# Kernel optimization log

Hardware: AMD Instinct MI355X
Metric: run time of the kernel (lower is better)

Reference implementation:

```python
import jax, jax.numpy as jnp
import numpy as np

B, L, ENC, DEC, EMB, ATT, V, T = 64, 196, 2048, 512, 512, 512, 20000, 26


def setup_inputs() -> dict:
    key = jax.random.key(0)
    ks = jax.random.split(key, 24)
    W = lambda i, shape: (jax.random.normal(ks[i], shape, dtype=jnp.float32) * 0.02)
    inp = {
        'encoder_output': jax.random.normal(ks[0], (B, L, ENC), dtype=jnp.float32),
        'caption': jax.random.randint(ks[1], (B, T), 0, V),
        'caption_lengths': jax.random.randint(ks[2], (B,), 2, T + 1),
        # embedding (uniform(-0.1,0.1) as in init_weights)
        'embed_W': jax.random.uniform(ks[3], (V, EMB), jnp.float32, -0.1, 0.1),
        # attention
        'We': W(4, (ENC, ATT)), 'be': jnp.zeros((ATT,), jnp.float32),
        'Wd': W(5, (DEC, ATT)), 'bd': jnp.zeros((ATT,), jnp.float32),
        'Wa': W(6, (ATT,)),     'ba': jnp.zeros((), jnp.float32),
        # LSTMCell (i,f,g,o order)
        'Wih': W(7, (4 * DEC, ENC + EMB)), 'bih': jnp.zeros((4 * DEC,), jnp.float32),
        'Whh': W(8, (4 * DEC, DEC)),       'bhh': jnp.zeros((4 * DEC,), jnp.float32),
        # gating + state init + output fc
        'Wfb': W(9, (DEC, ENC)),  'bfb': jnp.zeros((ENC,), jnp.float32),
        'Wh0': W(10, (ENC, DEC)), 'bh0': jnp.zeros((DEC,), jnp.float32),
        'Wc0': W(11, (ENC, DEC)), 'bc0': jnp.zeros((DEC,), jnp.float32),
        'Wfc': jax.random.uniform(ks[12], (DEC, V), jnp.float32, -0.1, 0.1),
        'bfc': jnp.zeros((V,), jnp.float32),
    }
    return inp


def _forward(encoder_output, caption, caption_lengths, embed_W, We, be, Wd, bd,
             Wa, ba, Wih, bih, Whh, bhh, Wfb, bfb, Wh0, bh0, Wc0, bc0, Wfc, bfc):
    # sort batch by descending caption length (as in the torch code)
    sort_ind = jnp.argsort(-caption_lengths)
    enc = encoder_output[sort_ind]          # [B, L, ENC]
    cap = caption[sort_ind]                 # [B, T]
    lens = caption_lengths[sort_ind] - 1    # decode steps per row

    emb = embed_W[cap]                      # [B, T, EMB]
    mean = enc.mean(axis=1)
    h0 = jnp.tanh(mean @ Wh0 + bh0)         # [B, DEC]
    c0 = jnp.tanh(mean @ Wc0 + bc0)
    enc_att = enc @ We + be                 # [B, L, ATT] (precomputed once)

    Tm1 = cap.shape[1] - 1
    # mask[t, b] = row b still active at step t
    mask = (jnp.arange(Tm1)[:, None] < lens[None, :]).astype(enc.dtype)  # [T-1, B]
    emb_steps = jnp.swapaxes(emb[:, :Tm1], 0, 1)                          # [T-1, B, EMB]

    def step(carry, x):
        h, c = carry
        e_t, m = x                                    # [B, EMB], [B]
        dec_att = h @ Wd + bd                         # [B, ATT]
        u = jnp.tanh(enc_att + dec_att[:, None, :])   # [B, L, ATT]
        scores = u @ Wa + ba                          # [B, L]
        alpha = jax.nn.softmax(scores, axis=1)
        z = jnp.einsum('bl,ble->be', alpha, enc)      # context [B, ENC]
        gate = jax.nn.sigmoid(h @ Wfb + bfb)          # [B, ENC]
        inp = jnp.concatenate([e_t, gate * z], axis=1)
        g = inp @ Wih.T + bih + h @ Whh.T + bhh       # [B, 4*DEC]
        i, f, gg, o = jnp.split(g, 4, axis=1)
        c_new = jax.nn.sigmoid(f) * c + jax.nn.sigmoid(i) * jnp.tanh(gg)
        h_new = jax.nn.sigmoid(o) * jnp.tanh(c_new)
        pred = h_new @ Wfc + bfc                      # [B, V]  (deep_output_layer == fc(h))
        return (h_new, c_new), (pred * m[:, None], alpha * m[:, None])

    _, (preds, alphas) = jax.lax.scan(step, (h0, c0), (emb_steps, mask))
    preds = jnp.swapaxes(preds, 0, 1)    # [B, T-1, V]
    alphas = jnp.swapaxes(alphas, 0, 1)  # [B, T-1, L]
    return preds, alphas, cap, lens


def reference(encoder_output, caption, caption_lengths, embed_W, We, be, Wd, bd,
              Wa, ba, Wih, bih, Whh, bhh, Wfb, bfb, Wh0, bh0, Wc0, bc0, Wfc, bfc):
    return _forward(encoder_output, caption, caption_lengths, embed_W, We, be, Wd, bd,
                    Wa, ba, Wih, bih, Whh, bhh, Wfb, bfb, Wh0, bh0, Wc0, bc0, Wfc, bfc)
```

## Files before the change

kernel.cpp:

```cpp
#include <hip/hip_runtime.h>
#include <hip/hip_bf16.h>

#define BB 64
#define LL 196
#define ENC 2048
#define DEC 512
#define EMB 512
#define ATT 512
#define VV 20000
#define TT 26
#define TM1 25

typedef __attribute__((ext_vector_type(8))) short bf16x8;
typedef __attribute__((ext_vector_type(4))) short bf16x4;
typedef __attribute__((ext_vector_type(4))) float f32x4;

#define MFMA16(a,b,c) __builtin_amdgcn_mfma_f32_16x16x32_bf16(a,b,c,0,0,0)

typedef const __attribute__((address_space(1))) void g_void;
typedef __attribute__((address_space(3))) void l_void;

__device__ __forceinline__ void stage16(const void* g, void* l){
    __builtin_amdgcn_global_load_lds((g_void*)g, (l_void*)l, 16, 0, 0);
}

#define WAITV(N) asm volatile("s_waitcnt vmcnt(" #N ")" ::: "memory")
#define PHASE_SYNC() do { __builtin_amdgcn_s_barrier(); __builtin_amdgcn_sched_barrier(0); } while(0)

__device__ __forceinline__ float tanh_fast(float x){
    float ax = fabsf(x);
    float e  = __expf(-2.f*ax);
    float r  = (1.f - e)/(1.f + e);
    return x >= 0.f ? r : -r;
}
__device__ __forceinline__ float sigmoidf_(float x){
    return 1.f/(1.f + __expf(-x));
}
__device__ __forceinline__ short f2bf(float v){
    __hip_bfloat16 b = __float2bfloat16(v);
    return __builtin_bit_cast(short, b);
}
__device__ __forceinline__ float bf2f(short s){
    __hip_bfloat16 b = __builtin_bit_cast(__hip_bfloat16, s);
    return __bfloat162float(b);
}

__global__ void k_sort(const int* __restrict__ clen, const int* __restrict__ cap,
                       const float* __restrict__ bih, const float* __restrict__ bhh,
                       int* __restrict__ sind, int* __restrict__ lens_s,
                       float* __restrict__ bsum,
                       float* __restrict__ out_cap, float* __restrict__ out_lens)
{
    int i = threadIdx.x;
    int li = clen[i];
    int r = 0;
    for (int j = 0; j < BB; j++){
        int lj = clen[j];
        r += (lj > li) || (lj == li && j < i);
    }
    sind[r] = i;
    lens_s[r] = li - 1;
    out_lens[r] = (float)(li - 1);
    for (int t = 0; t < TT; t++)
        out_cap[r*TT + t] = (float)cap[i*TT + t];
    for (int j = i; j < 4*DEC; j += BB)
        bsum[j] = bih[j] + bhh[j];
}

struct PrepArgs {
    const float* enc; const int* sind; short* enc_s;
    const float* Wfc; short* Wfcb;
    const float* Wih; const float* Whh; short* Bg;
    const float* We;  short* Web;
    const float* Wfb; short* Bfb;
    const float* Wd;  short* Wdp;
    float* mean;
    const float* embW; const int* cap; short* embs;
    int fast; int blkoff;
};

#define SEG0 12544
#define SEG1 (SEG0 + 5000)
#define SEG2 (SEG1 + 2560)
#define SEG3 (SEG2 + 512)
#define SEG4 (SEG3 + 512)
#define SEG5 (SEG4 + 512)
#define SEG6 (SEG5 + 512)
#define SEG7 (SEG6 + 1600)
#define SEG8 (SEG7 + 128)

__device__ __forceinline__ void pack_frag(int idx, const float* src, int ld,
                                          int K, int N, short* dst,
                                          int ktOff, int ntOff, int ntTot, bool NK)
{
    int ntCnt = N >> 4, ktCnt = K >> 5;
    int lane = idx & 63, rest = idx >> 6;
    if (rest >= ktCnt*ntCnt) return;
    int nt = rest % ntCnt, kt = rest / ntCnt;
    int k = kt*32 + (lane>>4)*8, n = nt*16 + (lane&15);
    bf16x8 v;
    #pragma unroll
    for (int j = 0; j < 8; j++){
        float f = NK ? src[(size_t)n*ld + k + j] : src[(size_t)(k+j)*ld + n];
        v[j] = f2bf(f);
    }
    *(bf16x8*)(dst + ((size_t)((kt+ktOff)*ntTot + (nt+ntOff))*64 + lane)*8) = v;
}

__launch_bounds__(256)
__global__ void k_prep(PrepArgs P)
{
    int blk = blockIdx.x + P.blkoff, tid = threadIdx.x;
    if (blk < SEG0){
        if (!P.fast) return;
        size_t idx = ((size_t)blk*256 + tid)*8;
        int r = (int)(idx / (LL*ENC));
        size_t rem = idx - (size_t)r*(LL*ENC);
        const float* s = P.enc + (size_t)P.sind[r]*(LL*ENC) + rem;
        bf16x8 v;
        float4 f0 = *(const float4*)s, f1 = *(const float4*)(s+4);
        v[0]=f2bf(f0.x); v[1]=f2bf(f0.y); v[2]=f2bf(f0.z); v[3]=f2bf(f0.w);
        v[4]=f2bf(f1.x); v[5]=f2bf(f1.y); v[6]=f2bf(f1.z); v[7]=f2bf(f1.w);
        *(bf16x8*)(P.enc_s + idx) = v;
    } else if (blk < SEG1){
        pack_frag((blk-SEG0)*256 + tid, P.Wfc, VV, 512, VV, P.Wfcb, 0, 0, 1250, false);
    } else if (blk < SEG2){
        pack_frag((blk-SEG1)*256 + tid, P.Wih, 2560, 2560, 2048, P.Bg, 0, 0, 128, true);
    } else if (blk < SEG3){
        pack_frag((blk-SEG2)*256 + tid, P.We, ATT, ENC, ATT, P.Web, 0, 0, 32, false);
    } else if (blk < SEG4){
        pack_frag((blk-SEG3)*256 + tid, P.Wfb, ENC, 512, 2048, P.Bfb, 0, 0, 128, false);
    } else if (blk < SEG5){
        pack_frag((blk-SEG4)*256 + tid, P.Whh, 512, 512, 2048, P.Bg, 80, 0, 128, true);
    } else if (blk < SEG6){
        int rel = blk - SEG5;
        int b = rel >> 3;
        int e = (rel & 7)*256 + tid;
        int sb = P.sind[b];
        const float* p = P.enc + ((size_t)sb*LL)*ENC + e;
        float s = 0.f;
        for (int l = 0; l < LL; l++) s += p[(size_t)l*ENC];
        P.mean[b*ENC + e] = s * (1.f/(float)LL);
    } else if (blk < SEG7){
        int rel = blk - SEG6;
        int b = rel / 25, t = rel % 25;
        int token = P.cap[P.sind[b]*TT + t];
        const float* src = P.embW + (size_t)token*EMB + tid*2;
        unsigned u = (unsigned)(unsigned short)f2bf(src[0]) |
                     ((unsigned)(unsigned short)f2bf(src[1]) << 16);
        ((unsigned*)(P.embs + ((size_t)b*TM1 + t)*EMB))[tid] = u;
    } else if (blk < SEG8){
        pack_frag((blk-SEG7)*256 + tid, P.Wd, ATT, 512, 512, P.Wdp, 0, 0, 32, false);
    }
}

#define KT 32
__launch_bounds__(256)
__global__ void k_h0part(const float* __restrict__ A1, const float* __restrict__ B1,
                         const float* __restrict__ B2, float* __restrict__ hpart)
{
    __shared__ float As[KT][64];
    __shared__ float Bs[KT][64];
    const int tid = threadIdx.x;
    const int n0  = blockIdx.x*64;
    const int kq  = blockIdx.y;
    float acc[4][4] = {};
    const int lrow = tid >> 3, lcol = tid & 7;
    const int bn = (tid & 15)*4, bk = tid >> 4;
    const int bi0 = (tid >> 4)*4, nj0 = (tid & 15)*4;
    for (int k0 = kq*256; k0 < kq*256 + 256; k0 += KT){
        #pragma unroll
        for (int p = 0; p < 2; p++){
            int m = lrow + p*32;
            float4 v = *(const float4*)(A1 + (size_t)m*2048 + k0 + lcol*4);
            As[lcol*4+0][m] = v.x; As[lcol*4+1][m] = v.y;
            As[lcol*4+2][m] = v.z; As[lcol*4+3][m] = v.w;
        }
        {
            bool hi = (n0 >= 512);
            const float* B = hi ? B2 : B1;
            int ncol = n0 - (hi ? 512 : 0) + bn;
            #pragma unroll
            for (int p = 0; p < 2; p++){
                int k = bk + p*16;
                *(float4*)&Bs[k][bn] = *(const float4*)(B + (size_t)(k0+k)*512 + ncol);
            }
        }
        __syncthreads();
        #pragma unroll
        for (int k = 0; k < KT; k++){
            const float4 av = *(const float4*)&As[k][bi0];
            const float4 bv = *(const float4*)&Bs[k][nj0];
            acc[0][0] += av.x*bv.x; acc[0][1] += av.x*bv.y; acc[0][2] += av.x*bv.z; acc[0][3] += av.x*bv.w;
            acc[1][0] += av.y*bv.x; acc[1][1] += av.y*bv.y; acc[1][2] += av.y*bv.z; acc[1][3] += av.y*bv.w;
            acc[2][0] += av.z*bv.x; acc[2][1] += av.z*bv.y; acc[2][2] += av.z*bv.z; acc[2][3] += av.z*bv.w;
            acc[3][0] += av.w*bv.x; acc[3][1] += av.w*bv.y; acc[3][2] += av.w*bv.z; acc[3][3] += av.w*bv.w;
        }
        __syncthreads();
    }
    #pragma unroll
    for (int i = 0; i < 4; i++)
        #pragma unroll
        for (int j = 0; j < 4; j++){
            int b = bi0 + i, n = n0 + nj0 + j;
            hpart[((size_t)kq*64 + b)*1024 + n] = acc[i][j];
        }
}

__global__ void k_h0fin(const float* __restrict__ hpart, const float* __restrict__ bh0,
                        const float* __restrict__ bc0, short* __restrict__ h0,
                        float* __restrict__ c)
{
    int idx = blockIdx.x*256 + threadIdx.x;
    int b = idx >> 10, n = idx & 1023;
    float v = (n < 512) ? bh0[n] : bc0[n-512];
    for (int kq = 0; kq < 8; kq++) v += hpart[((size_t)kq*64 + b)*1024 + n];
    float r = tanh_fast(v);
    if (n < 512) h0[b*512 + n] = f2bf(r);
    else         c[b*512 + (n-512)] = r;
}

template<bool BF16SRC>
__launch_bounds__(256)
__global__ void k_encatt_mfma(const void* __restrict__ encp, const int* __restrict__ sind,
                              const short* __restrict__ Web, const float* __restrict__ be,
                              short* __restrict__ enc_att)
{
    __shared__ short As[64*32];
    int tid = threadIdx.x, wv = tid>>6, lane = tid&63;
    int hi = lane>>4, lo = lane&15;
    int m0 = blockIdx.x*64;
    int ntbase = blockIdx.y*8 + wv*2;
    int srow = tid>>2, schunk = tid&3;
    const short* gsrcB = nullptr; const float* gsrcF = nullptr;
    if (BF16SRC){
        gsrcB = (const short*)encp + (size_t)(m0+srow)*ENC + schunk*8;
    } else {
        int grow = m0 + srow;
        int b = grow/LL, l = grow - b*LL;
        gsrcF = (const float*)encp + ((size_t)sind[b]*LL + l)*ENC + schunk*8;
    }
    int sws = srow*32 + (schunk ^ ((srow>>1)&3))*8;
    f32x4 acc[2][4] = {};
    for (int kt = 0; kt < 64; kt++){
        bf16x8 v;
        if (BF16SRC){
            v = *(const bf16x8*)(gsrcB + kt*32);
        } else {
            float4 f0 = *(const float4*)(gsrcF + kt*32);
            float4 f1 = *(const float4*)(gsrcF + kt*32 + 4);
            v[0]=f2bf(f0.x); v[1]=f2bf(f0.y); v[2]=f2bf(f0.z); v[3]=f2bf(f0.w);
            v[4]=f2bf(f1.x); v[5]=f2bf(f1.y); v[6]=f2bf(f1.z); v[7]=f2bf(f1.w);
        }
        __syncthreads();
        *(bf16x8*)(As + sws) = v;
        __syncthreads();
        bf16x8 af[4];
        #pragma unroll
        for (int m = 0; m < 4; m++){
            int r = m*16 + lo;
            af[m] = *(const bf16x8*)(As + r*32 + (hi ^ ((r>>1)&3))*8);
        }
        #pragma unroll
        for (int n = 0; n < 2; n++){
            bf16x8 b = *(const bf16x8*)(Web + ((size_t)(kt*32 + ntbase + n)*64 + lane)*8);
            #pragma unroll
            for (int m = 0; m < 4; m++)
                acc[n][m] = MFMA16(af[m], b, acc[n][m]);
        }
    }
    #pragma unroll
    for (int n = 0; n < 2; n++)
        #pragma unroll
        for (int m = 0; m < 4; m++)
            #pragma unroll
            for (int j = 0; j < 4; j++){
                int row = m0 + m*16 + hi*4 + j;
                int col = (ntbase + n)*16 + lo;
                enc_att[(size_t)row*ATT + col] = f2bf(acc[n][m][j] + be[col]);
            }
}

__launch_bounds__(256)
__global__ void k_hgemm(const short* __restrict__ h_in, const short* __restrict__ Wdp,
                        const short* __restrict__ Bfb,
                        const float* __restrict__ bd, const float* __restrict__ bfb,
                        float* __restrict__ dg, float* __restrict__ gateb)
{
    __shared__ short ring[4*16384];
    int tid = threadIdx.x, wv = tid>>6, lane = tid&63;
    int hi = lane>>4, lo = lane&15;
    int gw = blockIdx.x*4 + wv;
    bool isdg = (gw < 32);
    int ntl  = isdg ? gw : gw - 32;
    int bstr = isdg ? 32 : 128;
    const short* Bp = isdg ? Wdp : Bfb;
    int srow = tid>>2;
    int swc  = (tid&3) ^ ((srow>>1)&3);
    int swz  = (hi ^ ((lo>>1)&3))*8;
    auto STG = [&](int q){
        short* buf = ring + q*16384;
        #pragma unroll
        for (int j = 0; j < 4; j++){
            int kt = 4*q + j;
            stage16(h_in + (size_t)srow*512 + kt*32 + swc*8,
                    buf + j*2048 + wv*512);
            stage16(Bp + ((size_t)(kt*bstr + ntl)*64 + lane)*8,
                    buf + 8192 + wv*2048 + j*512);
        }
    };
    STG(0); STG(1); STG(2);
    f32x4 acc[4] = {};
    auto CMP = [&](int pp){
        const short* buf = ring + pp*16384;
        #pragma unroll
        for (int j = 0; j < 4; j++){
            bf16x8 b = *(const bf16x8*)(buf + 8192 + wv*2048 + j*512 + lane*8);
            const short* Ab = buf + j*2048;
            #pragma unroll
            for (int m = 0; m < 4; m++){
                bf16x8 a = *(const bf16x8*)(Ab + (m*16 + lo)*32 + swz);
                acc[m] = MFMA16(a, b, acc[m]);
            }
        }
    };
    WAITV(16); PHASE_SYNC(); STG(3); CMP(0);
    WAITV(16); PHASE_SYNC(); CMP(1);
    WAITV(8);  PHASE_SYNC(); CMP(2);
    WAITV(0);  PHASE_SYNC(); CMP(3);
    int col = ntl*16 + lo;
    if (isdg){
        #pragma unroll
        for (int m = 0; m < 4; m++)
            #pragma unroll
            for (int j = 0; j < 4; j++)
                dg[(m*16 + hi*4 + j)*512 + col] = acc[m][j] + bd[col];
    } else {
        #pragma unroll
        for (int m = 0; m < 4; m++)
            #pragma unroll
            for (int j = 0; j < 4; j++)
                gateb[(m*16 + hi*4 + j)*2048 + col] = sigmoidf_(acc[m][j] + bfb[col]);
    }
}

__launch_bounds__(512)
__global__ void k_attnz(const float* __restrict__ dg, const short* __restrict__ encat,
                        const float* __restrict__ Wa, const float* __restrict__ ba,
                        const short* __restrict__ embs, const float* __restrict__ gateb,
                        const short* __restrict__ enc_s, const float* __restrict__ enc,
                        const int* __restrict__ sind, const int* __restrict__ lens_s,
                        short* __restrict__ inp, float* __restrict__ out_alphas,
                        int t, int fast)
{
    __shared__ float da[512];
    __shared__ float was[512];
    __shared__ float sc[200];
    __shared__ float red[16];
    __shared__ float al[200];
    __shared__ float zpart[4*2048];
    int b = blockIdx.x, tid = threadIdx.x;
    int lane = tid & 63, wv = tid >> 6;
    da[tid] = dg[b*512 + tid];
    was[tid] = Wa[tid];
    __syncthreads();
    float ba_v = ba[0];
    for (int l = wv; l < LL; l += 8){
        const short* ea = encat + ((size_t)b*LL + l)*ATT;
        float s = 0.f;
        #pragma unroll
        for (int q = 0; q < 8; q++){
            int a = lane + q*64;
            s += tanh_fast(bf2f(ea[a]) + da[a]) * was[a];
        }
        #pragma unroll
        for (int off = 32; off; off >>= 1) s += __shfl_xor(s, off);
        if (lane == 0) sc[l] = s + ba_v;
    }
    __syncthreads();
    float v = -1e30f, e = 0.f;
    if (tid < 256){
        v = (tid < LL) ? sc[tid] : -1e30f;
        float mx = v;
        #pragma unroll
        for (int off = 32; off; off >>= 1) mx = fmaxf(mx, __shfl_xor(mx, off));
        if (lane == 0) red[wv] = mx;
    }
    if (tid < 256){
        const unsigned* s32 = (const unsigned*)(embs + ((size_t)b*TM1 + t)*EMB);
        ((unsigned*)(inp + (size_t)b*2560))[tid] = s32[tid];
    }
    __syncthreads();
    float mxa = fmaxf(fmaxf(red[0], red[1]), fmaxf(red[2], red[3]));
    if (tid < 256){
        e = (tid < LL) ? __expf(v - mxa) : 0.f;
        float sm = e;
        #pragma unroll
        for (int off = 32; off; off >>= 1) sm += __shfl_xor(sm, off);
        if (lane == 0) red[8 + wv] = sm;
    }
    __syncthreads();
    float tot = red[8] + red[9] + red[10] + red[11];
    if (tid < LL){
        float alv = e / tot;
        al[tid] = alv;
        float m = (t < lens_s[b]) ? 1.f : 0.f;
        out_alphas[((size_t)b*TM1 + t)*LL + tid] = alv * m;
    }
    __syncthreads();
    {
        int ls = tid >> 7;
        int cs = tid & 127;
        int c0 = cs*16;
        float a16[16] = {};
        if (fast){
            const short* base = enc_s + ((size_t)b*LL)*ENC + c0;
            for (int l = ls; l < LL; l += 4){
                float av = al[l];
                const short* r = base + (size_t)l*ENC;
                bf16x8 v0 = *(const bf16x8*)(r);
                bf16x8 v1 = *(const bf16x8*)(r + 8);
                #pragma unroll
                for (int j = 0; j < 8; j++){
                    a16[j]     += av*bf2f(v0[j]);
                    a16[8 + j] += av*bf2f(v1[j]);
                }
            }
        } else {
            const float* base = enc + ((size_t)sind[b]*LL)*ENC + c0;
            for (int l = ls; l < LL; l += 4){
                float av = al[l];
                const float* r = base + (size_t)l*ENC;
                float4 f0 = *(const float4*)(r),     f1 = *(const float4*)(r+4);
                float4 f2 = *(const float4*)(r + 8), f3 = *(const float4*)(r+12);
                a16[0]+=av*f0.x; a16[1]+=av*f0.y; a16[2]+=av*f0.z; a16[3]+=av*f0.w;
                a16[4]+=av*f1.x; a16[5]+=av*f1.y; a16[6]+=av*f1.z; a16[7]+=av*f1.w;
                a16[8]+=av*f2.x; a16[9]+=av*f2.y; a16[10]+=av*f2.z; a16[11]+=av*f2.w;
                a16[12]+=av*f3.x; a16[13]+=av*f3.y; a16[14]+=av*f3.z; a16[15]+=av*f3.w;
            }
        }
        float* zp = zpart + ls*2048 + c0;
        #pragma unroll
        for (int jj = 0; jj < 16; jj++){
            int slot = (jj + cs) & 15;
            zp[slot] = a16[slot];
        }
    }
    __syncthreads();
    {
        int c = tid*4;
        const float* gt = gateb + (size_t)b*2048 + c;
        bf16x4 o;
        #pragma unroll
        for (int j = 0; j < 4; j++){
            float s = zpart[0*2048 + c + j] + zpart[1*2048 + c + j]
                    + zpart[2*2048 + c + j] + zpart[3*2048 + c + j];
            o[j] = f2bf(gt[j] * s);
        }
        *(bf16x4*)(inp + (size_t)b*2560 + 512 + c) = o;
    }
}

__launch_bounds__(512)
__global__ void k_glstm(const short* __restrict__ inp, const short* __restrict__ h_in,
                        const short* __restrict__ Bg, const float* __restrict__ bsum,
                        float* __restrict__ c, short* __restrict__ h_out)
{
    __shared__ short ring[3*24576];
    float* gs = (float*)ring;
    int tid = threadIdx.x, wv = tid>>6, lane = tid&63;
    int hi = lane>>4, lo = lane&15;
    int gate = wv & 3, khalf = wv >> 2;
    int j16 = blockIdx.x;
    int nt = gate*32 + j16;
    int sl   = tid >> 8;
    int st   = tid & 255;
    int srow = st >> 2;
    int swc  = (st&3) ^ ((srow>>1)&3);
    int swz  = (hi ^ ((lo>>1)&3))*8;
    auto STG = [&](int q){
        short* buf = ring + (q%3)*24576;
        #pragma unroll
        for (int j = 0; j < 3; j++){
            int kt = sl*48 + 3*q + j;
            const short* src;
            if (kt < 80) src = inp  + (size_t)srow*2560 + kt*32 + swc*8;
            else         src = h_in + (size_t)srow*512  + (kt-80)*32 + swc*8;
            stage16(src, buf + (sl*3 + j)*2048 + (wv&3)*512);
            int ktw = khalf*48 + 3*q + j;
            stage16(Bg + ((size_t)(ktw*128 + nt)*64 + lane)*8,
                    buf + 12288 + wv*1536 + j*512);
        }
    };
    STG(0); STG(1);
    f32x4 acc[4] = {};
    auto CMP = [&](int pp){
        const short* buf = ring + (pp%3)*24576;
        #pragma unroll
        for (int j = 0; j < 3; j++){
            bf16x8 b = *(const bf16x8*)(buf + 12288 + wv*1536 + j*512 + lane*8);
            const short* Ab = buf + (khalf*3 + j)*2048;
            #pragma unroll
            for (int m = 0; m < 4; m++){
                bf16x8 a = *(const bf16x8*)(Ab + (m*16 + lo)*32 + swz);
                acc[m] = MFMA16(a, b, acc[m]);
            }
        }
    };
    for (int pp = 0; pp < 14; pp++){
        WAITV(6); PHASE_SYNC();
        STG(pp + 2);
        CMP(pp);
    }
    WAITV(6); PHASE_SYNC(); CMP(14);
    WAITV(0); PHASE_SYNC(); CMP(15);
    __syncthreads();
    #pragma unroll
    for (int m = 0; m < 4; m++)
        #pragma unroll
        for (int j = 0; j < 4; j++)
            gs[wv*1088 + (m*16 + hi*4 + j)*17 + lo] = acc[m][j];
    __syncthreads();
    #pragma unroll
    for (int rep = 0; rep < 2; rep++){
        int idx = rep*512 + tid;
        int row = idx >> 4, cl = idx & 15;
        int col = j16*16 + cl;
        float s0 = gs[0*1088 + row*17 + cl] + gs[4*1088 + row*17 + cl] + bsum[col];
        float s1 = gs[1*1088 + row*17 + cl] + gs[5*1088 + row*17 + cl] + bsum[512 + col];
        float s2 = gs[2*1088 + row*17 + cl] + gs[6*1088 + row*17 + cl] + bsum[1024 + col];
        float s3 = gs[3*1088 + row*17 + cl] + gs[7*1088 + row*17 + cl] + bsum[1536 + col];
        int ci = row*512 + col;
        float cn = sigmoidf_(s1)*c[ci] + sigmoidf_(s0)*tanh_fast(s2);
        c[ci] = cn;
        h_out[ci] = f2bf(sigmoidf_(s3)*tanh_fast(cn));
    }
}

__launch_bounds__(256)
__global__ void k_predall(const short* __restrict__ hh, const short* __restrict__ Wfcb,
                          const float* __restrict__ bfc, const int* __restrict__ lens_s,
                          float* __restrict__ out_preds)
{
    __shared__ short ring[4*2048];
    int tid = threadIdx.x, wv = tid>>6, lane = tid&63;
    int hi = lane>>4, lo = lane&15;
    int nt = blockIdx.x*4 + wv;
    if (nt > 1249) nt = 1249;
    int mt0 = blockIdx.y*5;
    bf16x8 breg[16];
    #pragma unroll
    for (int kt = 0; kt < 16; kt++)
        breg[kt] = *(const bf16x8*)(Wfcb + ((size_t)(kt*1250 + nt)*64 + lane)*8);
    int col = nt*16 + lo;
    float bv = bfc[col];
    int lv[16];
    #pragma unroll
    for (int m = 0; m < 4; m++)
        #pragma unroll
        for (int j = 0; j < 4; j++)
            lv[m*4 + j] = lens_s[m*16 + hi*4 + j];

    int srow = tid>>2;
    int swc  = (tid&3) ^ ((srow>>1)&3);
    int swz  = (hi ^ ((lo>>1)&3))*8;
    const short* hh0 = hh + (size_t)(mt0 + 1)*(BB*DEC);
    auto STG = [&](int q){
        const short* src = hh0 + (size_t)(q>>4)*(BB*DEC) + (size_t)srow*512
                         + (q&15)*32 + swc*8;
        stage16(src, ring + (q&3)*2048 + wv*512);
    };
    STG(0); STG(1); STG(2);

    auto CMP = [&](f32x4* acc, int kt, int pp){
        const short* base = ring + (pp&3)*2048;
        #pragma unroll
        for (int m = 0; m < 4; m++){
            bf16x8 a = *(const bf16x8*)(base + (m*16 + lo)*32 + swz);
            acc[m] = MFMA16(a, breg[kt], acc[m]);
        }
    };
    auto STORE = [&](f32x4* acc, int mta){
        #pragma unroll
        for (int m = 0; m < 4; m++)
            #pragma unroll
            for (int j = 0; j < 4; j++){
                int row = m*16 + hi*4 + j;
                float mk = (mta < lv[m*4 + j]) ? 1.f : 0.f;
                out_preds[((size_t)row*TM1 + mta)*VV + col] = mk*(acc[m][j] + bv);
            }
    };

    for (int mt = 0; mt < 4; mt++){
        f32x4 acc[4] = {};
        #pragma unroll
        for (int kt = 0; kt < 16; kt++){
            int pp = mt*16 + kt;
            WAITV(2); PHASE_SYNC();
            STG(pp + 3);
            CMP(acc, kt, pp);
        }
        STORE(acc, mt0 + mt);
    }
    {
        f32x4 acc[4] = {};
        #pragma unroll
        for (int kt = 0; kt < 13; kt++){
            int pp = 64 + kt;
            WAITV(2); PHASE_SYNC();
            if (pp < 77) STG(pp + 3);
            CMP(acc, kt, pp);
        }
        WAITV(2); PHASE_SYNC(); CMP(acc, 13, 77);
        WAITV(1); PHASE_SYNC(); CMP(acc, 14, 78);
        WAITV(0); PHASE_SYNC(); CMP(acc, 15, 79);
        STORE(acc, mt0 + 4);
    }
}

extern "C" void kernel_launch(void* const* d_in, const int* in_sizes, int n_in,
                              void* d_out, int out_size, void* d_ws, size_t ws_size,
                              hipStream_t stream)
{
    const float* enc  = (const float*)d_in[0];
    const int*   cap  = (const int*)  d_in[1];
    const int*   clen = (const int*)  d_in[2];
    const float* embW = (const float*)d_in[3];
    const float* We   = (const float*)d_in[4];
    const float* be   = (const float*)d_in[5];
    const float* Wd   = (const float*)d_in[6];
    const float* bd   = (const float*)d_in[7];
    const float* Wa   = (const float*)d_in[8];
    const float* ba   = (const float*)d_in[9];
    const float* Wih  = (const float*)d_in[10];
    const float* bih  = (const float*)d_in[11];
    const float* Whh  = (const float*)d_in[12];
    const float* bhh  = (const float*)d_in[13];
    const float* Wfb  = (const float*)d_in[14];
    const float* bfb  = (const float*)d_in[15];
    const float* Wh0  = (const float*)d_in[16];
    const float* bh0  = (const float*)d_in[17];
    const float* Wc0  = (const float*)d_in[18];
    const float* bc0  = (const float*)d_in[19];
    const float* Wfc  = (const float*)d_in[20];
    const float* bfc  = (const float*)d_in[21];

    char* w = (char*)d_ws;
    size_t cur = 0;
    auto alloc = [&](size_t bytes)->char*{
        char* p = w + cur; cur = (cur + bytes + 255) & ~(size_t)255; return p;
    };
    int*   sind   = (int*)  alloc(256);
    int*   lens_s = (int*)  alloc(256);
    float* bsum   = (float*)alloc(4*DEC*4);
    float* mean   = (float*)alloc(BB*ENC*4);
    float* hpart  = (float*)alloc((size_t)8*64*1024*4);
    float* c      = (float*)alloc(BB*DEC*4);
    short* hh     = (short*)alloc((size_t)(TM1+1)*BB*DEC*2);
    float* dg     = (float*)alloc(BB*512*4);
    float* gateb  = (float*)alloc(BB*2048*4);
    short* inp    = (short*)alloc(BB*2560*2);
    short* embs   = (short*)alloc((size_t)BB*TM1*EMB*2);
    short* Wdp    = (short*)alloc((size_t)512*512*2);
    short* Web    = (short*)alloc((size_t)ENC*ATT*2);
    short* Bfb    = (short*)alloc((size_t)512*2048*2);
    short* Bg     = (short*)alloc((size_t)3072*2048*2);
    short* Wfcb   = (short*)alloc((size_t)512*VV*2);
    short* encat  = (short*)alloc((size_t)BB*LL*ATT*2);
    short* enc_s  = (short*)alloc((size_t)BB*LL*ENC*2);
    bool fast = (ws_size >= cur);
    int fastI = fast ? 1 : 0;

    float* out        = (float*)d_out;
    float* out_preds  = out;
    float* out_alphas = out + 32000000ull;
    float* out_cap    = out + 32313600ull;
    float* out_lens   = out + 32315264ull;

    k_sort<<<1, 64, 0, stream>>>(clen, cap, bih, bhh, sind, lens_s, bsum,
                                 out_cap, out_lens);
    PrepArgs P;
    P.enc = enc; P.sind = sind; P.enc_s = enc_s;
    P.Wfc = Wfc; P.Wfcb = Wfcb;
    P.Wih = Wih; P.Whh = Whh; P.Bg = Bg;
    P.We = We; P.Web = Web;
    P.Wfb = Wfb; P.Bfb = Bfb;
    P.Wd = Wd; P.Wdp = Wdp;
    P.mean = mean;
    P.embW = embW; P.cap = cap; P.embs = embs;
    P.fast = fastI;
    P.blkoff = 0;
    k_prep<<<SEG0, 256, 0, stream>>>(P);
    PrepArgs P2 = P;
    P2.blkoff = SEG0;
    k_prep<<<SEG8 - SEG0, 256, 0, stream>>>(P2);

    k_h0part<<<dim3(16, 8), 256, 0, stream>>>(mean, Wh0, Wc0, hpart);
    k_h0fin<<<256, 256, 0, stream>>>(hpart, bh0, bc0, hh, c);

    if (fast)
        k_encatt_mfma<true ><<<dim3(196, 4), 256, 0, stream>>>(enc_s, sind, Web, be, encat);
    else
        k_encatt_mfma<false><<<dim3(196, 4), 256, 0, stream>>>(enc,   sind, Web, be, encat);

    for (int t = 0; t < TM1; t++){
        const short* h_in  = hh + (size_t)t*(BB*DEC);
        short*       h_out = hh + (size_t)(t+1)*(BB*DEC);
        k_hgemm<<<40, 256, 0, stream>>>(h_in, Wdp, Bfb, bd, bfb, dg, gateb);
        k_attnz<<<64, 512, 0, stream>>>(dg, encat, Wa, ba, embs, gateb, enc_s, enc,
                                        sind, lens_s, inp, out_alphas, t, fastI);
        k_glstm<<<32, 512, 0, stream>>>(inp, h_in, Bg, bsum, c, h_out);
    }
    k_predall<<<dim3(313, 5), 256, 0, stream>>>(hh, Wfcb, bfc, lens_s, out_preds);
}
```

Before: 1.856 ms.

## Fuse per-step decoder and gate GEMMs into attention kernel, dropping k_hgemm

```diff
diff --git a/kernel.cpp b/kernel.cpp
--- a/kernel.cpp
+++ b/kernel.cpp
@@ -72,8 +72,6 @@
     const float* Wfc; short* Wfcb;
     const float* Wih; const float* Whh; short* Bg;
     const float* We;  short* Web;
-    const float* Wfb; short* Bfb;
-    const float* Wd;  short* Wdp;
     float* mean;
     const float* embW; const int* cap; short* embs;
     int fast; int blkoff;
@@ -85,9 +83,7 @@
 #define SEG3 (SEG2 + 512)
 #define SEG4 (SEG3 + 512)
 #define SEG5 (SEG4 + 512)
-#define SEG6 (SEG5 + 512)
-#define SEG7 (SEG6 + 1600)
-#define SEG8 (SEG7 + 128)
+#define SEG6 (SEG5 + 1600)
 
 __device__ __forceinline__ void pack_frag(int idx, const float* src, int ld,
                                           int K, int N, short* dst,
@@ -129,11 +125,9 @@
     } else if (blk < SEG3){
         pack_frag((blk-SEG2)*256 + tid, P.We, ATT, ENC, ATT, P.Web, 0, 0, 32, false);
     } else if (blk < SEG4){
-        pack_frag((blk-SEG3)*256 + tid, P.Wfb, ENC, 512, 2048, P.Bfb, 0, 0, 128, false);
+        pack_frag((blk-SEG3)*256 + tid, P.Whh, 512, 512, 2048, P.Bg, 80, 0, 128, true);
     } else if (blk < SEG5){
-        pack_frag((blk-SEG4)*256 + tid, P.Whh, 512, 512, 2048, P.Bg, 80, 0, 128, true);
-    } else if (blk < SEG6){
-        int rel = blk - SEG5;
+        int rel = blk - SEG4;
         int b = rel >> 3;
         int e = (rel & 7)*256 + tid;
         int sb = P.sind[b];
@@ -141,16 +135,14 @@
         float s = 0.f;
         for (int l = 0; l < LL; l++) s += p[(size_t)l*ENC];
         P.mean[b*ENC + e] = s * (1.f/(float)LL);
-    } else if (blk < SEG7){
-        int rel = blk - SEG6;
+    } else if (blk < SEG6){
+        int rel = blk - SEG5;
         int b = rel / 25, t = rel % 25;
         int token = P.cap[P.sind[b]*TT + t];
         const float* src = P.embW + (size_t)token*EMB + tid*2;
         unsigned u = (unsigned)(unsigned short)f2bf(src[0]) |
                      ((unsigned)(unsigned short)f2bf(src[1]) << 16);
         ((unsigned*)(P.embs + ((size_t)b*TM1 + t)*EMB))[tid] = u;
-    } else if (blk < SEG8){
-        pack_frag((blk-SEG7)*256 + tid, P.Wd, ATT, 512, 512, P.Wdp, 0, 0, 32, false);
     }
 }
 
@@ -281,78 +273,19 @@
             }
 }
 
-__launch_bounds__(256)
-__global__ void k_hgemm(const short* __restrict__ h_in, const short* __restrict__ Wdp,
-                        const short* __restrict__ Bfb,
-                        const float* __restrict__ bd, const float* __restrict__ bfb,
-                        float* __restrict__ dg, float* __restrict__ gateb)
-{
-    __shared__ short ring[4*16384];
-    int tid = threadIdx.x, wv = tid>>6, lane = tid&63;
-    int hi = lane>>4, lo = lane&15;
-    int gw = blockIdx.x*4 + wv;
-    bool isdg = (gw < 32);
-    int ntl  = isdg ? gw : gw - 32;
-    int bstr = isdg ? 32 : 128;
-    const short* Bp = isdg ? Wdp : Bfb;
-    int srow = tid>>2;
-    int swc  = (tid&3) ^ ((srow>>1)&3);
-    int swz  = (hi ^ ((lo>>1)&3))*8;
-    auto STG = [&](int q){
-        short* buf = ring + q*16384;
-        #pragma unroll
-        for (int j = 0; j < 4; j++){
-            int kt = 4*q + j;
-            stage16(h_in + (size_t)srow*512 + kt*32 + swc*8,
-                    buf + j*2048 + wv*512);
-            stage16(Bp + ((size_t)(kt*bstr + ntl)*64 + lane)*8,
-                    buf + 8192 + wv*2048 + j*512);
-        }
-    };
-    STG(0); STG(1); STG(2);
-    f32x4 acc[4] = {};
-    auto CMP = [&](int pp){
-        const short* buf = ring + pp*16384;
-        #pragma unroll
-        for (int j = 0; j < 4; j++){
-            bf16x8 b = *(const bf16x8*)(buf + 8192 + wv*2048 + j*512 + lane*8);
-            const short* Ab = buf + j*2048;
-            #pragma unroll
-            for (int m = 0; m < 4; m++){
-                bf16x8 a = *(const bf16x8*)(Ab + (m*16 + lo)*32 + swz);
-                acc[m] = MFMA16(a, b, acc[m]);
-            }
-        }
-    };
-    WAITV(16); PHASE_SYNC(); STG(3); CMP(0);
-    WAITV(16); PHASE_SYNC(); CMP(1);
-    WAITV(8);  PHASE_SYNC(); CMP(2);
-    WAITV(0);  PHASE_SYNC(); CMP(3);
-    int col = ntl*16 + lo;
-    if (isdg){
-        #pragma unroll
-        for (int m = 0; m < 4; m++)
-            #pragma unroll
-            for (int j = 0; j < 4; j++)
-                dg[(m*16 + hi*4 + j)*512 + col] = acc[m][j] + bd[col];
-    } else {
-        #pragma unroll
-        for (int m = 0; m < 4; m++)
-            #pragma unroll
-            for (int j = 0; j < 4; j++)
-                gateb[(m*16 + hi*4 + j)*2048 + col] = sigmoidf_(acc[m][j] + bfb[col]);
-    }
-}
-
 __launch_bounds__(512)
-__global__ void k_attnz(const float* __restrict__ dg, const short* __restrict__ encat,
-                        const float* __restrict__ Wa, const float* __restrict__ ba,
-                        const short* __restrict__ embs, const float* __restrict__ gateb,
-                        const short* __restrict__ enc_s, const float* __restrict__ enc,
-                        const int* __restrict__ sind, const int* __restrict__ lens_s,
-                        short* __restrict__ inp, float* __restrict__ out_alphas,
-                        int t, int fast)
-{
+__global__ void k_attnz2(const short* __restrict__ h_in,
+                         const float* __restrict__ Wd, const float* __restrict__ bd,
+                         const float* __restrict__ Wfb, const float* __restrict__ bfb,
+                         const short* __restrict__ encat,
+                         const float* __restrict__ Wa, const float* __restrict__ ba,
+                         const short* __restrict__ embs,
+                         const short* __restrict__ enc_s, const float* __restrict__ enc,
+                         const int* __restrict__ sind, const int* __restrict__ lens_s,
+                         short* __restrict__ inp, float* __restrict__ out_alphas,
+                         int t, int fast)
+{
+    __shared__ float hf[512];
     __shared__ float da[512];
     __shared__ float was[512];
     __shared__ float sc[200];
@@ -361,9 +294,29 @@
     __shared__ float zpart[4*2048];
     int b = blockIdx.x, tid = threadIdx.x;
     int lane = tid & 63, wv = tid >> 6;
-    da[tid] = dg[b*512 + tid];
+
+    hf[tid] = bf2f(h_in[b*512 + tid]);
     was[tid] = Wa[tid];
-    __syncthreads();
+    if (tid < 256){
+        const unsigned* s32 = (const unsigned*)(embs + ((size_t)b*TM1 + t)*EMB);
+        ((unsigned*)(inp + (size_t)b*2560))[tid] = s32[tid];
+    }
+    __syncthreads();
+
+    {
+        const float* Wcol = Wd + tid;
+        float a0 = 0.f, a1 = 0.f, a2 = 0.f, a3 = 0.f;
+        for (int k = 0; k < 512; k += 4){
+            float4 h4 = *(const float4*)&hf[k];
+            a0 += h4.x * Wcol[(size_t)(k+0)*ATT];
+            a1 += h4.y * Wcol[(size_t)(k+1)*ATT];
+            a2 += h4.z * Wcol[(size_t)(k+2)*ATT];
+            a3 += h4.w * Wcol[(size_t)(k+3)*ATT];
+        }
+        da[tid] = (a0 + a1) + (a2 + a3) + bd[tid];
+    }
+    __syncthreads();
+
     float ba_v = ba[0];
     for (int l = wv; l < LL; l += 8){
         const short* ea = encat + ((size_t)b*LL + l)*ATT;
@@ -385,10 +338,6 @@
         #pragma unroll
         for (int off = 32; off; off >>= 1) mx = fmaxf(mx, __shfl_xor(mx, off));
         if (lane == 0) red[wv] = mx;
-    }
-    if (tid < 256){
-        const unsigned* s32 = (const unsigned*)(embs + ((size_t)b*TM1 + t)*EMB);
-        ((unsigned*)(inp + (size_t)b*2560))[tid] = s32[tid];
     }
     __syncthreads();
     float mxa = fmaxf(fmaxf(red[0], red[1]), fmaxf(red[2], red[3]));
@@ -407,7 +356,26 @@
         float m = (t < lens_s[b]) ? 1.f : 0.f;
         out_alphas[((size_t)b*TM1 + t)*LL + tid] = alv * m;
     }
-    __syncthreads();
+
+    float g4[4];
+    {
+        int c0 = tid*4;
+        const float* Wg = Wfb + c0;
+        float4 acc0 = {0.f,0.f,0.f,0.f}, acc1 = {0.f,0.f,0.f,0.f};
+        for (int k = 0; k < 512; k += 2){
+            float4 w0 = *(const float4*)&Wg[(size_t)(k+0)*ENC];
+            float4 w1 = *(const float4*)&Wg[(size_t)(k+1)*ENC];
+            float hv0 = hf[k], hv1 = hf[k+1];
+            acc0.x += hv0*w0.x; acc0.y += hv0*w0.y; acc0.z += hv0*w0.z; acc0.w += hv0*w0.w;
+            acc1.x += hv1*w1.x; acc1.y += hv1*w1.y; acc1.z += hv1*w1.z; acc1.w += hv1*w1.w;
+        }
+        g4[0] = sigmoidf_(acc0.x + acc1.x + bfb[c0+0]);
+        g4[1] = sigmoidf_(acc0.y + acc1.y + bfb[c0+1]);
+        g4[2] = sigmoidf_(acc0.z + acc1.z + bfb[c0+2]);
+        g4[3] = sigmoidf_(acc0.w + acc1.w + bfb[c0+3]);
+    }
+    __syncthreads();
+
     {
         int ls = tid >> 7;
         int cs = tid & 127;
@@ -449,13 +417,12 @@
     __syncthreads();
     {
         int c = tid*4;
-        const float* gt = gateb + (size_t)b*2048 + c;
         bf16x4 o;
         #pragma unroll
         for (int j = 0; j < 4; j++){
             float s = zpart[0*2048 + c + j] + zpart[1*2048 + c + j]
                     + zpart[2*2048 + c + j] + zpart[3*2048 + c + j];
-            o[j] = f2bf(gt[j] * s);
+            o[j] = f2bf(g4[j] * s);
         }
         *(bf16x4*)(inp + (size_t)b*2560 + 512 + c) = o;
     }
@@ -657,13 +624,9 @@
     float* hpart  = (float*)alloc((size_t)8*64*1024*4);
     float* c      = (float*)alloc(BB*DEC*4);
     short* hh     = (short*)alloc((size_t)(TM1+1)*BB*DEC*2);
-    float* dg     = (float*)alloc(BB*512*4);
-    float* gateb  = (float*)alloc(BB*2048*4);
     short* inp    = (short*)alloc(BB*2560*2);
     short* embs   = (short*)alloc((size_t)BB*TM1*EMB*2);
-    short* Wdp    = (short*)alloc((size_t)512*512*2);
     short* Web    = (short*)alloc((size_t)ENC*ATT*2);
-    short* Bfb    = (short*)alloc((size_t)512*2048*2);
     short* Bg     = (short*)alloc((size_t)3072*2048*2);
     short* Wfcb   = (short*)alloc((size_t)512*VV*2);
     short* encat  = (short*)alloc((size_t)BB*LL*ATT*2);
@@ -684,8 +647,6 @@
     P.Wfc = Wfc; P.Wfcb = Wfcb;
     P.Wih = Wih; P.Whh = Whh; P.Bg = Bg;
     P.We = We; P.Web = Web;
-    P.Wfb = Wfb; P.Bfb = Bfb;
-    P.Wd = Wd; P.Wdp = Wdp;
     P.mean = mean;
     P.embW = embW; P.cap = cap; P.embs = embs;
     P.fast = fastI;
@@ -693,7 +654,7 @@
     k_prep<<<SEG0, 256, 0, stream>>>(P);
     PrepArgs P2 = P;
     P2.blkoff = SEG0;
-    k_prep<<<SEG8 - SEG0, 256, 0, stream>>>(P2);
+    k_prep<<<SEG6 - SEG0, 256, 0, stream>>>(P2);
 
     k_h0part<<<dim3(16, 8), 256, 0, stream>>>(mean, Wh0, Wc0, hpart);
     k_h0fin<<<256, 256, 0, stream>>>(hpart, bh0, bc0, hh, c);
@@ -706,9 +667,9 @@
     for (int t = 0; t < TM1; t++){
         const short* h_in  = hh + (size_t)t*(BB*DEC);
         short*       h_out = hh + (size_t)(t+1)*(BB*DEC);
-        k_hgemm<<<40, 256, 0, stream>>>(h_in, Wdp, Bfb, bd, bfb, dg, gateb);
-        k_attnz<<<64, 512, 0, stream>>>(dg, encat, Wa, ba, embs, gateb, enc_s, enc,
-                                        sind, lens_s, inp, out_alphas, t, fastI);
+        k_attnz2<<<64, 512, 0, stream>>>(h_in, Wd, bd, Wfb, bfb, encat, Wa, ba,
+                                         embs, enc_s, enc, sind, lens_s,
+                                         inp, out_alphas, t, fastI);
         k_glstm<<<32, 512, 0, stream>>>(inp, h_in, Bg, bsum, c, h_out);
     }
     k_predall<<<dim3(313, 5), 256, 0, stream>>>(hh, Wfcb, bfc, lens_s, out_preds);
```

After: 2.891 ms. 1.56x slower.
